# Performance work log

Measured on AMD Instinct MI355X. Metric: run time of the kernel, lower is better.

Reference implementation:

```python
import jax, jax.numpy as jnp
import numpy as np

# norse LIFCell default constants
DT = 1e-3
TAU_SYN_INV = 200.0
TAU_MEM_INV = 100.0
V_TH = 1.0
ALPHA = 100.0  # SuperSpike surrogate slope
BN_EPS = 1e-5
DECAY = 0.995

@jax.custom_vjp
def spike_fn(x):
    return (x > 0).astype(x.dtype)

def _spike_fwd(x):
    return spike_fn(x), x

def _spike_bwd(x, g):
    return (g / (ALPHA * jnp.abs(x) + 1.0) ** 2,)

spike_fn.defvjp(_spike_fwd, _spike_bwd)

def bn(x, g, b, m, v):
    return (x - m) * jax.lax.rsqrt(v + BN_EPS) * g + b

def lif_step(inp, v, i):
    # explicit Euler LIF update (v_leak = v_reset = 0)
    v_dec = v + DT * TAU_MEM_INV * (-v + i)
    i_dec = i * (1.0 - DT * TAU_SYN_INV)
    z = spike_fn(v_dec - V_TH)
    v_new = (1.0 - z) * v_dec
    i_new = i_dec + inp
    return z, v_new, i_new

def setup_inputs() -> dict:
    key = jax.random.key(0)
    ks = jax.random.split(key, 8)
    B, F, T = 2048, 512, 100
    H1, H2, H3, O = 1024, 512, 256, 2
    def xavier(k, fan_out, fan_in):
        lim = np.sqrt(6.0 / (fan_in + fan_out)).astype(np.float32)
        return jax.random.uniform(k, (fan_out, fan_in), jnp.float32, -lim, lim)
    def bn_params(k, n):
        return dict(g=jax.random.uniform(k, (n,), jnp.float32, 0.5, 1.5),
                    b=jnp.zeros((n,), jnp.float32),
                    m=jnp.zeros((n,), jnp.float32),
                    v=jnp.ones((n,), jnp.float32))
    bni = bn_params(ks[1], F); bn1 = bn_params(ks[2], H1)
    bn2 = bn_params(ks[3], H2); bn3 = bn_params(ks[4], H3)
    return {
        "x": jax.random.normal(ks[0], (B, F, T), jnp.float32),
        "bni_g": bni["g"], "bni_b": bni["b"], "bni_m": bni["m"], "bni_v": bni["v"],
        "W1": xavier(ks[5], H1, F), "b1": jnp.zeros((H1,), jnp.float32),
        "bn1_g": bn1["g"], "bn1_b": bn1["b"], "bn1_m": bn1["m"], "bn1_v": bn1["v"],
        "W2": xavier(ks[6], H2, H1), "b2": jnp.zeros((H2,), jnp.float32),
        "bn2_g": bn2["g"], "bn2_b": bn2["b"], "bn2_m": bn2["m"], "bn2_v": bn2["v"],
        "W3": xavier(ks[7], H3, H2), "b3": jnp.zeros((H3,), jnp.float32),
        "bn3_g": bn3["g"], "bn3_b": bn3["b"], "bn3_m": bn3["m"], "bn3_v": bn3["v"],
        "Wout": xavier(jax.random.fold_in(key, 99), O, H3),
        "bout": jnp.zeros((O,), jnp.float32),
    }

def reference(x, bni_g, bni_b, bni_m, bni_v,
              W1, b1, bn1_g, bn1_b, bn1_m, bn1_v,
              W2, b2, bn2_g, bn2_b, bn2_m, bn2_v,
              W3, b3, bn3_g, bn3_b, bn3_m, bn3_v,
              Wout, bout):
    B, F, T = x.shape
    O = Wout.shape[0]
    xs = jnp.moveaxis(x, 2, 0)  # (T, B, F)
    weights = DECAY ** jnp.arange(T - 1, -1, -1, dtype=x.dtype)  # (T,)

    def step(carry, inp):
        (v1, i1, v2, i2, v3, i3, vo, io, acc) = carry
        x_t, w = inp
        h = bn(x_t, bni_g, bni_b, bni_m, bni_v)
        c1 = bn(h @ W1.T + b1, bn1_g, bn1_b, bn1_m, bn1_v)
        z1, v1, i1 = lif_step(c1, v1, i1)
        c2 = bn(z1 @ W2.T + b2, bn2_g, bn2_b, bn2_m, bn2_v)
        z2, v2, i2 = lif_step(c2, v2, i2)
        c3 = bn(z2 @ W3.T + b3, bn3_g, bn3_b, bn3_m, bn3_v)
        z3, v3, i3 = lif_step(c3, v3, i3)
        co = z3 @ Wout.T + bout
        zo, vo, io = lif_step(co, vo, io)
        acc = acc + zo * w
        return (v1, i1, v2, i2, v3, i3, vo, io, acc), None

    zf = lambda n: jnp.zeros((B, n), x.dtype)
    init = (zf(W1.shape[0]), zf(W1.shape[0]), zf(W2.shape[0]), zf(W2.shape[0]),
            zf(W3.shape[0]), zf(W3.shape[0]), zf(O), zf(O), zf(O))
    carry, _ = jax.lax.scan(step, init, (xs, weights))
    return carry[-1]
```

## Files before the change

### kernel.cpp

```cpp
#include <hip/hip_runtime.h>
#include <cmath>

#define BATCH 2048
#define FDIM  512
#define TDIM  100
#define H1    1024
#define H2    512
#define H3    256
#define ODIM  2
#define TC    20
#define NCH   5
#define CHM   (TC * BATCH)

typedef __attribute__((ext_vector_type(8))) _Float16 f16x8;
typedef __attribute__((ext_vector_type(4))) _Float16 f16x4;
typedef __attribute__((ext_vector_type(4))) float f32x4;
typedef __attribute__((ext_vector_type(4))) int i32x4;

struct W20 { float w[TC]; };

__device__ __forceinline__ void gl16(const void* g, void* l) {
  __builtin_amdgcn_global_load_lds(
      (const __attribute__((address_space(1))) unsigned int*)g,
      (__attribute__((address_space(3))) unsigned int*)l, 16, 0, 0);
}

__device__ __forceinline__ void lif_update(float c, float& v, float& i, float& z) {
  float vd = v + 0.1f * (i - v);
  float id = 0.8f * i;
  z = (vd - 1.0f) > 0.0f ? 1.0f : 0.0f;
  v = (z != 0.0f) ? 0.0f : vd;
  i = id + c;
}

__global__ void zero_kernel(float* __restrict__ p, int n) {
  for (int i = blockIdx.x * blockDim.x + threadIdx.x; i < n; i += gridDim.x * blockDim.x)
    p[i] = 0.0f;
}

__global__ void tchunk_kernel(const float* __restrict__ x, _Float16* __restrict__ xp, int t0) {
  __shared__ float tile[64][21];
  const int b = blockIdx.y;
  const int f0 = blockIdx.x * 64;
  const int tid = threadIdx.x;
  {
    const int f = tid / 5, tq = tid % 5;
    float4 v = *reinterpret_cast<const float4*>(
        &x[(size_t)b * FDIM * TDIM + (size_t)(f0 + f) * TDIM + t0 + tq * 4]);
    tile[f][tq * 4 + 0] = v.x; tile[f][tq * 4 + 1] = v.y;
    tile[f][tq * 4 + 2] = v.z; tile[f][tq * 4 + 3] = v.w;
  }
  __syncthreads();
  {
    const int t = tid >> 4;
    const int fq = tid & 15;
    const size_t PS = (size_t)CHM * FDIM;
    f16x4 h, m;
    #pragma unroll
    for (int j = 0; j < 4; ++j) {
      float xa = tile[fq * 4 + j][t] * 64.0f;
      _Float16 hh = (_Float16)xa;
      float rm = (xa - (float)hh) * 4096.0f;
      h[j] = hh;
      m[j] = (_Float16)rm;
    }
    const size_t o = ((size_t)t * BATCH + b) * FDIM + f0 + fq * 4;
    *reinterpret_cast<f16x4*>(&xp[o])      = h;
    *reinterpret_cast<f16x4*>(&xp[PS + o]) = m;
  }
}

__global__ void fold1_f16(const float* __restrict__ W1, const float* __restrict__ b1,
                          const float* __restrict__ g1, const float* __restrict__ bb1,
                          const float* __restrict__ m1, const float* __restrict__ v1,
                          const float* __restrict__ gi, const float* __restrict__ bi,
                          const float* __restrict__ mi, const float* __restrict__ vi,
                          _Float16* __restrict__ W1p, float* __restrict__ s1,
                          float* __restrict__ e1) {
  __shared__ float swf[FDIM];
  __shared__ float red[8];
  __shared__ float bsw[1];
  const int j = blockIdx.x, tid = threadIdx.x;
  const float sg = g1[j] / sqrtf(v1[j] + 1e-5f);
  float part = 0.0f, pmax = 0.0f;
  for (int f = tid; f < FDIM; f += 256) {
    float si = gi[f] / sqrtf(vi[f] + 1e-5f);
    float h0 = bi[f] - mi[f] * si;
    float w  = W1[j * FDIM + f];
    part += w * h0;
    float wf = w * si * sg;
    swf[f] = wf;
    pmax = fmaxf(pmax, fabsf(wf));
  }
  #pragma unroll
  for (int s = 1; s < 64; s <<= 1) {
    part += __shfl_xor(part, s);
    pmax = fmaxf(pmax, __shfl_xor(pmax, s));
  }
  if ((tid & 63) == 0) { red[tid >> 6] = part; red[4 + (tid >> 6)] = pmax; }
  __syncthreads();
  if (tid == 0) {
    float d = red[0] + red[1] + red[2] + red[3];
    e1[j] = (d + b1[j] - m1[j]) * sg + bb1[j];
    float mx = fmaxf(fmaxf(red[4], red[5]), fmaxf(red[6], red[7]));
    int e = 0;
    if (mx > 0.0f) frexpf(mx, &e);
    s1[j] = exp2f((float)(e - 11));
    bsw[0] = exp2f((float)(5 - e));
  }
  __syncthreads();
  const float SW = bsw[0];
  const size_t PS = (size_t)H1 * FDIM;
  for (int f = tid; f < FDIM; f += 256) {
    float wa = swf[f] * SW;
    _Float16 wh = (_Float16)wa;
    float r = (wa - (float)wh) * 4096.0f;
    W1p[(size_t)j * FDIM + f]      = wh;
    W1p[PS + (size_t)j * FDIM + f] = (_Float16)r;
  }
}

__global__ void foldS_i8(const float* __restrict__ W, const float* __restrict__ b,
                         const float* __restrict__ g, const float* __restrict__ bb,
                         const float* __restrict__ m, const float* __restrict__ v,
                         signed char* __restrict__ Wq, float* __restrict__ qs,
                         float* __restrict__ e, int N, int K) {
  __shared__ float swf[1024];
  __shared__ float red[4];
  __shared__ int bse[1];
  const int j = blockIdx.x, tid = threadIdx.x;
  const float sg = g[j] / sqrtf(v[j] + 1e-5f);
  float pmax = 0.0f;
  for (int k = tid; k < K; k += 256) {
    float wf = W[(size_t)j * K + k] * sg;
    swf[k] = wf;
    pmax = fmaxf(pmax, fabsf(wf));
  }
  #pragma unroll
  for (int s = 1; s < 64; s <<= 1) pmax = fmaxf(pmax, __shfl_xor(pmax, s));
  if ((tid & 63) == 0) red[tid >> 6] = pmax;
  __syncthreads();
  if (tid == 0) {
    float mx = fmaxf(fmaxf(red[0], red[1]), fmaxf(red[2], red[3]));
    int ee = 0;
    if (mx > 0.0f) frexpf(mx, &ee);
    qs[j] = exp2f((float)(ee - 27));
    bse[0] = 27 - ee;
    e[j] = (b[j] - m[j]) * sg + bb[j];
  }
  __syncthreads();
  const double sc = ldexp(1.0, bse[0]);
  const size_t PS = (size_t)N * K;
  for (int k = tid; k < K; k += 256) {
    long D = llround((double)swf[k] * sc);
    #pragma unroll
    for (int p = 0; p < 3; p++) {
      int d = (int)(D & 127);
      if (d >= 64) d -= 128;
      Wq[(size_t)p * PS + (size_t)j * K + k] = (signed char)d;
      D = (D - d) >> 7;
    }
    Wq[3 * PS + (size_t)j * K + k] = (signed char)D;
  }
}

__global__ __launch_bounds__(256, 2)
void g1c_kernel(const _Float16* __restrict__ A, const _Float16* __restrict__ Wp,
                const float* __restrict__ s1, const float* __restrict__ e1,
                float* __restrict__ cOut)
{
  constexpr int BM = 128, BN = 64, K = FDIM, N = H1, BK = 64;
  constexpr int FR = 4, FC = 2, WTM = 64, WTN = 32;
  __shared__ __align__(16) _Float16 As[2][BM][BK];
  __shared__ __align__(16) _Float16 Bs[2][BN][BK];
  const int tid = threadIdx.x, lane = tid & 63, wid = tid >> 6;
  const int wr = wid >> 1, wc = wid & 1;
  const int l16 = lane & 15, lq = lane >> 4;
  const int bnk = blockIdx.x, bmk = blockIdx.y;
  const size_t APS = (size_t)CHM * FDIM;
  const size_t WPS = (size_t)N * K;
  const int lrow8 = lane >> 3, lslot = lane & 7;

  f32x4 accA[FR][FC] = {}, accB[FR][FC] = {};

  auto stage = [&](int it) {
    const int k0 = it * BK;
    #pragma unroll
    for (int q = 0; q < 8; ++q) {
      int i = q * 4 + wid;
      int s = i >> 4, r0 = (i & 15) * 8;
      int row = r0 + lrow8;
      int ss = lslot ^ (row & 7);
      gl16(A + (size_t)s * APS + (size_t)(bmk * BM + row) * K + k0 + ss * 8, &As[s][r0][0]);
    }
    #pragma unroll
    for (int q = 0; q < 4; ++q) {
      int i = q * 4 + wid;
      int s = i >> 3, r0 = (i & 7) * 8;
      int row = r0 + lrow8;
      int ss = lslot ^ (row & 7);
      gl16(Wp + (size_t)s * WPS + (size_t)(bnk * BN + row) * K + k0 + ss * 8, &Bs[s][r0][0]);
    }
  };

  auto loadA = [&](int kh, int s, int fr) -> f16x8 {
    int row = wr * WTM + fr * 16 + l16;
    int slot = ((kh << 2) | lq) ^ (row & 7);
    return *reinterpret_cast<const f16x8*>(&As[s][row][slot * 8]);
  };
  auto loadB = [&](int kh, int s, int fc) -> f16x8 {
    int row = wc * WTN + fc * 16 + l16;
    int slot = ((kh << 2) | lq) ^ (row & 7);
    return *reinterpret_cast<const f16x8*>(&Bs[s][row][slot * 8]);
  };

  stage(0);
  __syncthreads();
  constexpr int NK = K / BK;
  for (int it = 0; it < NK; ++it) {
    {
      f16x8 af[2][FR], bf[2][FC];
      #pragma unroll
      for (int s = 0; s < 2; ++s) {
        #pragma unroll
        for (int fr = 0; fr < FR; ++fr) af[s][fr] = loadA(0, s, fr);
        #pragma unroll
        for (int fc = 0; fc < FC; ++fc) bf[s][fc] = loadB(0, s, fc);
      }
      #pragma unroll
      for (int fr = 0; fr < FR; ++fr)
        #pragma unroll
        for (int fc = 0; fc < FC; ++fc) {
          accA[fr][fc] = __builtin_amdgcn_mfma_f32_16x16x32_f16(af[0][fr], bf[0][fc], accA[fr][fc], 0, 0, 0);
          accB[fr][fc] = __builtin_amdgcn_mfma_f32_16x16x32_f16(af[0][fr], bf[1][fc], accB[fr][fc], 0, 0, 0);
          accB[fr][fc] = __builtin_amdgcn_mfma_f32_16x16x32_f16(af[1][fr], bf[0][fc], accB[fr][fc], 0, 0, 0);
        }
    }
    {
      f16x8 af[2][FR], bf[2][FC];
      #pragma unroll
      for (int s = 0; s < 2; ++s) {
        #pragma unroll
        for (int fr = 0; fr < FR; ++fr) af[s][fr] = loadA(1, s, fr);
        #pragma unroll
        for (int fc = 0; fc < FC; ++fc) bf[s][fc] = loadB(1, s, fc);
      }
      __syncthreads();
      if (it + 1 < NK) stage(it + 1);
      #pragma unroll
      for (int fr = 0; fr < FR; ++fr)
        #pragma unroll
        for (int fc = 0; fc < FC; ++fc) {
          accA[fr][fc] = __builtin_amdgcn_mfma_f32_16x16x32_f16(af[0][fr], bf[0][fc], accA[fr][fc], 0, 0, 0);
          accB[fr][fc] = __builtin_amdgcn_mfma_f32_16x16x32_f16(af[0][fr], bf[1][fc], accB[fr][fc], 0, 0, 0);
          accB[fr][fc] = __builtin_amdgcn_mfma_f32_16x16x32_f16(af[1][fr], bf[0][fc], accB[fr][fc], 0, 0, 0);
        }
      __syncthreads();
    }
  }

  #pragma unroll
  for (int fc = 0; fc < FC; ++fc) {
    const int n = bnk * BN + wc * WTN + fc * 16 + l16;
    const float eb = e1[n], sn = s1[n];
    #pragma unroll
    for (int fr = 0; fr < FR; ++fr) {
      const int row0 = bmk * BM + wr * WTM + fr * 16 + lq * 4;
      #pragma unroll
      for (int r = 0; r < 4; ++r)
        cOut[(size_t)(row0 + r) * N + n] =
            sn * (accA[fr][fc][r] + 0.000244140625f * accB[fr][fc][r]) + eb;
    }
  }
}

template<int BM, int BN>
__global__ __launch_bounds__(256, 2)
void gSc_kernel(const signed char* __restrict__ A, const signed char* __restrict__ Wq,
                const float* __restrict__ qs, const float* __restrict__ eb_,
                float* __restrict__ cOut, const int N, const int K)
{
  constexpr int BKI = 128;
  constexpr int WTM = BM / 2, WTN = BN / 2, FR = WTM / 16, FC = WTN / 16;
  constexpr int RA = BM / 8, RB = BN / 8;
  __shared__ __align__(16) signed char As[BM][BKI];
  __shared__ __align__(16) signed char Bs[4][BN][BKI];
  const int tid = threadIdx.x, lane = tid & 63, wid = tid >> 6;
  const int wr = wid >> 1, wc = wid & 1;
  const int l16 = lane & 15, lq = lane >> 4;
  const int bnk = blockIdx.x, bmk = blockIdx.y;
  const size_t WPS = (size_t)N * K;
  const int lrow8 = lane >> 3, lslot = lane & 7;

  i32x4 acc[4][FR][FC] = {};

  auto stage = [&](int it) {
    const int k0 = it * BKI;
    #pragma unroll
    for (int q = 0; q < RA / 4; ++q) {
      int i = q * 4 + wid;
      int r0 = i * 8, row = r0 + lrow8;
      int ss = lslot ^ (row & 7);
      gl16(A + (size_t)(bmk * BM + row) * K + k0 + ss * 16, &As[r0][0]);
    }
    #pragma unroll
    for (int q = 0; q < RB; ++q) {
      int i = q * 4 + wid;
      int s = i / RB, r0 = (i % RB) * 8, row = r0 + lrow8;
      int ss = lslot ^ (row & 7);
      gl16(Wq + (size_t)s * WPS + (size_t)(bnk * BN + row) * K + k0 + ss * 16, &Bs[s][r0][0]);
    }
  };

  auto loadA = [&](int kh, int fr) -> i32x4 {
    int row = wr * WTM + fr * 16 + l16;
    int slot = ((kh << 2) | lq) ^ (row & 7);
    return *reinterpret_cast<const i32x4*>(&As[row][slot * 16]);
  };
  auto loadB = [&](int kh, int s, int fc) -> i32x4 {
    int row = wc * WTN + fc * 16 + l16;
    int slot = ((kh << 2) | lq) ^ (row & 7);
    return *reinterpret_cast<const i32x4*>(&Bs[s][row][slot * 16]);
  };

  stage(0);
  __syncthreads();
  const int NK = K / BKI;
  for (int it = 0; it < NK; ++it) {
    {
      i32x4 av[FR], bv[4][FC];
      #pragma unroll
      for (int fr = 0; fr < FR; ++fr) av[fr] = loadA(0, fr);
      #pragma unroll
      for (int s = 0; s < 4; ++s)
        #pragma unroll
        for (int fc = 0; fc < FC; ++fc) bv[s][fc] = loadB(0, s, fc);
      #pragma unroll
      for (int s = 0; s < 4; ++s)
        #pragma unroll
        for (int fr = 0; fr < FR; ++fr)
          #pragma unroll
          for (int fc = 0; fc < FC; ++fc)
            acc[s][fr][fc] = __builtin_amdgcn_mfma_i32_16x16x64_i8(av[fr], bv[s][fc], acc[s][fr][fc], 0, 0, 0);
    }
    {
      i32x4 av[FR], bv[4][FC];
      #pragma unroll
      for (int fr = 0; fr < FR; ++fr) av[fr] = loadA(1, fr);
      #pragma unroll
      for (int s = 0; s < 4; ++s)
        #pragma unroll
        for (int fc = 0; fc < FC; ++fc) bv[s][fc] = loadB(1, s, fc);
      __syncthreads();
      if (it + 1 < NK) stage(it + 1);
      #pragma unroll
      for (int s = 0; s < 4; ++s)
        #pragma unroll
        for (int fr = 0; fr < FR; ++fr)
          #pragma unroll
          for (int fc = 0; fc < FC; ++fc)
            acc[s][fr][fc] = __builtin_amdgcn_mfma_i32_16x16x64_i8(av[fr], bv[s][fc], acc[s][fr][fc], 0, 0, 0);
      __syncthreads();
    }
  }

  #pragma unroll
  for (int fc = 0; fc < FC; ++fc) {
    const int n = bnk * BN + wc * WTN + fc * 16 + l16;
    const float qv = qs[n], eb = eb_[n];
    #pragma unroll
    for (int fr = 0; fr < FR; ++fr) {
      const int row0 = bmk * BM + wr * WTM + fr * 16 + lq * 4;
      #pragma unroll
      for (int r = 0; r < 4; ++r) {
        int slo = acc[0][fr][fc][r] + (acc[1][fr][fc][r] << 7) + (acc[2][fr][fc][r] << 14);
        cOut[(size_t)(row0 + r) * N + n] =
            qv * fmaf(2097152.0f, (float)acc[3][fr][fc][r], (float)slo) + eb;
      }
    }
  }
}

__global__ void scan_lif_kernel(const float* __restrict__ c, float* __restrict__ vst,
                                float* __restrict__ ist, signed char* __restrict__ z,
                                int NN)
{
  const int i4 = (blockIdx.x * 256 + threadIdx.x) * 4;
  float4 v  = *reinterpret_cast<const float4*>(&vst[i4]);
  float4 ii = *reinterpret_cast<const float4*>(&ist[i4]);
  for (int t = 0; t < TC; ++t) {
    const size_t o = (size_t)t * NN + i4;
    float4 cc = *reinterpret_cast<const float4*>(&c[o]);
    float4 zz;
    lif_update(cc.x, v.x, ii.x, zz.x);
    lif_update(cc.y, v.y, ii.y, zz.y);
    lif_update(cc.z, v.z, ii.z, zz.z);
    lif_update(cc.w, v.w, ii.w, zz.w);
    unsigned pz = (zz.x != 0.f ? 1u : 0u) | (zz.y != 0.f ? 256u : 0u)
                | (zz.z != 0.f ? 65536u : 0u) | (zz.w != 0.f ? 16777216u : 0u);
    *reinterpret_cast<unsigned*>(&z[o]) = pz;
  }
  *reinterpret_cast<float4*>(&vst[i4]) = v;
  *reinterpret_cast<float4*>(&ist[i4]) = ii;
}

__global__ void outc_kernel(const signed char* __restrict__ z3, const float* __restrict__ Wout,
                            const float* __restrict__ bout, float* __restrict__ vo,
                            float* __restrict__ io, float* __restrict__ out, W20 wts)
{
  const int tid = threadIdx.x;
  const int ks = tid & 15, p = tid >> 4;
  const int o = p & 1, bl = p >> 1;
  const int b = blockIdx.x * 8 + bl;
  float wv[16];
  const float* wbase = Wout + (size_t)o * H3 + ks * 16;
  #pragma unroll
  for (int j = 0; j < 16; ++j) wv[j] = wbase[j];
  const float bo = bout[o];
  const int sidx = b * ODIM + o;
  float v = vo[sidx], i = io[sidx], accl = 0.0f;
  for (int t = 0; t < TC; ++t) {
    const signed char* zr = z3 + ((size_t)t * BATCH + b) * H3 + ks * 16;
    i32x4 zw = *reinterpret_cast<const i32x4*>(zr);
    float s = 0.0f;
    #pragma unroll
    for (int j = 0; j < 16; ++j)
      s = fmaf((float)((zw[j >> 2] >> ((j & 3) * 8)) & 1), wv[j], s);
    s += __shfl_xor(s, 1); s += __shfl_xor(s, 2);
    s += __shfl_xor(s, 4); s += __shfl_xor(s, 8);
    float zo;
    lif_update(s + bo, v, i, zo);
    accl += zo * wts.w[t];
  }
  if (ks == 0) { vo[sidx] = v; io[sidx] = i; out[sidx] += accl; }
}

__global__ void fold1_kernel(const float* __restrict__ W1, const float* __restrict__ b1,
                             const float* __restrict__ g1, const float* __restrict__ bb1,
                             const float* __restrict__ m1, const float* __restrict__ v1,
                             const float* __restrict__ gi, const float* __restrict__ bi,
                             const float* __restrict__ mi, const float* __restrict__ vi,
                             float* __restrict__ W1f, float* __restrict__ e1) {
  const int j = blockIdx.x;
  const int tid = threadIdx.x;
  const float sg = g1[j] / sqrtf(v1[j] + 1e-5f);
  float part = 0.0f;
  for (int f = tid; f < FDIM; f += 256) {
    float si = gi[f] / sqrtf(vi[f] + 1e-5f);
    float h0 = bi[f] - mi[f] * si;
    float w  = W1[j * FDIM + f];
    part += w * h0;
    W1f[j * FDIM + f] = w * si * sg;
  }
  #pragma unroll
  for (int m = 1; m < 64; m <<= 1) part += __shfl_xor(part, m);
  __shared__ float red[4];
  if ((tid & 63) == 0) red[tid >> 6] = part;
  __syncthreads();
  if (tid == 0) {
    float d = red[0] + red[1] + red[2] + red[3];
    e1[j] = (d + b1[j] - m1[j]) * sg + bb1[j];
  }
}

__global__ void foldS_kernel(const float* __restrict__ W, const float* __restrict__ b,
                             const float* __restrict__ g, const float* __restrict__ bb,
                             const float* __restrict__ m, const float* __restrict__ v,
                             float* __restrict__ Wf, float* __restrict__ e, int K) {
  const int j = blockIdx.x;
  const float sg = g[j] / sqrtf(v[j] + 1e-5f);
  for (int k = threadIdx.x; k < K; k += 256)
    Wf[j * K + k] = W[j * K + k] * sg;
  if (threadIdx.x == 0) e[j] = (b[j] - m[j]) * sg + bb[j];
}

template<int TM, int TN, bool CONTIG>
__global__ __launch_bounds__(256, 2)
void gemm_lif_kernel(const float* __restrict__ A, size_t ars, size_t acs,
                     const float* __restrict__ W, const float* __restrict__ ebias,
                     float* __restrict__ vst, float* __restrict__ ist,
                     float* __restrict__ zout, int N, int K)
{
  constexpr int BK = 16;
  constexpr int BM = 16 * TM;
  constexpr int BN = 16 * TN;
  __shared__ float As[BK][BM];
  __shared__ float Bs[BK][BN];
  const int tid = threadIdx.x;
  const int tx = tid & 15, ty = tid >> 4;
  const int bn = blockIdx.x, bm = blockIdx.y;
  const float* Ablk = A + (size_t)bm * BM * ars;
  const float* Wblk = W + (size_t)bn * BN * (size_t)K;

  float acc[TM][TN];
  #pragma unroll
  for (int r = 0; r < TM; r++)
    #pragma unroll
    for (int c = 0; c < TN; c++) acc[r][c] = 0.0f;

  for (int k0 = 0; k0 < K; k0 += BK) {
    if (CONTIG) {
      constexpr int A4 = BM * BK / 4;
      #pragma unroll
      for (int q = 0; q < A4 / 256; q++) {
        int idx = q * 256 + tid;
        int r = idx >> 2;
        int kq = (idx & 3) << 2;
        float4 val = *reinterpret_cast<const float4*>(Ablk + (size_t)r * ars + (size_t)(k0 + kq));
        As[kq + 0][r] = val.x; As[kq + 1][r] = val.y;
        As[kq + 2][r] = val.z; As[kq + 3][r] = val.w;
      }
    } else {
      #pragma unroll
      for (int q = 0; q < BM * BK / 256; q++) {
        int idx = q * 256 + tid;
        int r = idx >> 4;
        int kk = idx & 15;
        As[kk][r] = Ablk[(size_t)r * ars + (size_t)(k0 + kk) * acs];
      }
    }
    {
      int n  = tid >> 2;
      int kq = (tid & 3) << 2;
      float4 val = *reinterpret_cast<const float4*>(Wblk + (size_t)n * K + (size_t)(k0 + kq));
      Bs[kq + 0][n] = val.x; Bs[kq + 1][n] = val.y;
      Bs[kq + 2][n] = val.z; Bs[kq + 3][n] = val.w;
    }
    __syncthreads();
    #pragma unroll
    for (int kk = 0; kk < BK; kk++) {
      float a[TM], bv[TN];
      const float4* ap = reinterpret_cast<const float4*>(&As[kk][ty * TM]);
      *reinterpret_cast<float4*>(&a[0]) = ap[0];
      if (TM == 8) *reinterpret_cast<float4*>(&a[4]) = ap[1];
      *reinterpret_cast<float4*>(&bv[0]) = *reinterpret_cast<const float4*>(&Bs[kk][tx * TN]);
      #pragma unroll
      for (int r = 0; r < TM; r++)
        #pragma unroll
        for (int c = 0; c < TN; c++)
          acc[r][c] = fmaf(a[r], bv[c], acc[r][c]);
    }
    __syncthreads();
  }

  const int n0 = bn * BN + tx * TN;
  const float4 ev = *reinterpret_cast<const float4*>(ebias + n0);
  #pragma unroll
  for (int r = 0; r < TM; r++) {
    const int brow = bm * BM + ty * TM + r;
    const size_t idx = (size_t)brow * N + n0;
    float c0 = acc[r][0] + ev.x;
    float c1 = acc[r][1] + ev.y;
    float c2 = acc[r][2] + ev.z;
    float c3 = acc[r][3] + ev.w;
    float4 vv = *reinterpret_cast<const float4*>(vst + idx);
    float4 ii = *reinterpret_cast<const float4*>(ist + idx);
    float4 zz;
    lif_update(c0, vv.x, ii.x, zz.x);
    lif_update(c1, vv.y, ii.y, zz.y);
    lif_update(c2, vv.z, ii.z, zz.z);
    lif_update(c3, vv.w, ii.w, zz.w);
    *reinterpret_cast<float4*>(zout + idx) = zz;
    *reinterpret_cast<float4*>(vst  + idx) = vv;
    *reinterpret_cast<float4*>(ist  + idx) = ii;
  }
}

__global__ void out_kernel(const float* __restrict__ z3, const float* __restrict__ Wout,
                           const float* __restrict__ bout, float* __restrict__ vo,
                           float* __restrict__ io, float* __restrict__ acc, float wt) {
  const int idx = blockIdx.x * 256 + threadIdx.x;
  if (idx >= BATCH * ODIM) return;
  const int b = idx >> 1, o = idx & 1;
  const float4* zr = reinterpret_cast<const float4*>(z3 + (size_t)b * H3);
  const float4* wr = reinterpret_cast<const float4*>(Wout + o * H3);
  float s = 0.0f;
  #pragma unroll 4
  for (int k = 0; k < H3 / 4; k++) {
    float4 zv = zr[k], wv = wr[k];
    s += zv.x * wv.x + zv.y * wv.y + zv.z * wv.z + zv.w * wv.w;
  }
  float cin = s + bout[o];
  float v = vo[idx], i = io[idx], z;
  lif_update(cin, v, i, z);
  vo[idx] = v; io[idx] = i;
  acc[idx] += z * wt;
}

extern "C" void kernel_launch(void* const* d_in, const int* in_sizes, int n_in,
                              void* d_out, int out_size, void* d_ws, size_t ws_size,
                              hipStream_t stream) {
  const float* x     = (const float*)d_in[0];
  const float* bni_g = (const float*)d_in[1];
  const float* bni_b = (const float*)d_in[2];
  const float* bni_m = (const float*)d_in[3];
  const float* bni_v = (const float*)d_in[4];
  const float* W1    = (const float*)d_in[5];
  const float* b1    = (const float*)d_in[6];
  const float* bn1_g = (const float*)d_in[7];
  const float* bn1_b = (const float*)d_in[8];
  const float* bn1_m = (const float*)d_in[9];
  const float* bn1_v = (const float*)d_in[10];
  const float* W2    = (const float*)d_in[11];
  const float* b2    = (const float*)d_in[12];
  const float* bn2_g = (const float*)d_in[13];
  const float* bn2_b = (const float*)d_in[14];
  const float* bn2_m = (const float*)d_in[15];
  const float* bn2_v = (const float*)d_in[16];
  const float* W3    = (const float*)d_in[17];
  const float* b3    = (const float*)d_in[18];
  const float* bn3_g = (const float*)d_in[19];
  const float* bn3_b = (const float*)d_in[20];
  const float* bn3_m = (const float*)d_in[21];
  const float* bn3_v = (const float*)d_in[22];
  const float* Wout  = (const float*)d_in[23];
  const float* bout  = (const float*)d_in[24];
  float* out = (float*)d_out;

  float* ws = (float*)d_ws;
  size_t off = 0;
  auto alloc = [&](size_t n) { float* p = ws + off; off += n; return p; };

  float* e1 = alloc(H1);
  float* e2 = alloc(H2);
  float* e3 = alloc(H3);
  float* s1 = alloc(H1);
  float* q2 = alloc(H2);
  float* q3 = alloc(H3);
  float* v1 = alloc((size_t)BATCH * H1);
  float* i1 = alloc((size_t)BATCH * H1);
  float* v2 = alloc((size_t)BATCH * H2);
  float* i2 = alloc((size_t)BATCH * H2);
  float* v3 = alloc((size_t)BATCH * H3);
  float* i3 = alloc((size_t)BATCH * H3);
  float* vo = alloc((size_t)BATCH * ODIM);
  float* io = alloc((size_t)BATCH * ODIM);
  float* cbuf = alloc((size_t)CHM * H1);
  _Float16* hs = (_Float16*)(ws + off);
  size_t hoff = 0;
  _Float16* W1p = hs; hoff += (size_t)2 * H1 * FDIM;
  _Float16* Xp_c = hs + hoff; hoff += (size_t)2 * CHM * FDIM;
  signed char* za = (signed char*)Xp_c;
  signed char* bs = (signed char*)(hs + hoff);
  size_t boff = 0;
  signed char* W2q = bs + boff; boff += (size_t)4 * H2 * H1;
  signed char* W3q = bs + boff; boff += (size_t)4 * H3 * H2;
  const size_t needed = off * sizeof(float) + hoff * sizeof(_Float16) + boff;

  const int nstate = BATCH * (2 * H1 + 2 * H2 + 2 * H3 + 2 * ODIM);

  if (ws_size >= needed) {
    zero_kernel<<<2048, 256, 0, stream>>>(v1, nstate);
    zero_kernel<<<16, 256, 0, stream>>>(out, BATCH * ODIM);

    fold1_f16<<<H1, 256, 0, stream>>>(W1, b1, bn1_g, bn1_b, bn1_m, bn1_v,
                                      bni_g, bni_b, bni_m, bni_v, W1p, s1, e1);
    foldS_i8<<<H2, 256, 0, stream>>>(W2, b2, bn2_g, bn2_b, bn2_m, bn2_v, W2q, q2, e2, H2, H1);
    foldS_i8<<<H3, 256, 0, stream>>>(W3, b3, bn3_g, bn3_b, bn3_m, bn3_v, W3q, q3, e3, H3, H2);

    for (int ch = 0; ch < NCH; ++ch) {
      const int t0 = ch * TC;
      tchunk_kernel<<<dim3(FDIM / 64, BATCH), 320, 0, stream>>>(x, Xp_c, t0);
      g1c_kernel<<<dim3(H1 / 64, CHM / 128), 256, 0, stream>>>(Xp_c, W1p, s1, e1, cbuf);
      scan_lif_kernel<<<BATCH * H1 / 1024, 256, 0, stream>>>(cbuf, v1, i1, za, BATCH * H1);
      gSc_kernel<64, 64><<<dim3(H2 / 64, CHM / 64), 256, 0, stream>>>(za, W2q, q2, e2, cbuf, H2, H1);
      scan_lif_kernel<<<BATCH * H2 / 1024, 256, 0, stream>>>(cbuf, v2, i2, za, BATCH * H2);
      gSc_kernel<64, 32><<<dim3(H3 / 32, CHM / 64), 256, 0, stream>>>(za, W3q, q3, e3, cbuf, H3, H2);
      scan_lif_kernel<<<BATCH * H3 / 1024, 256, 0, stream>>>(cbuf, v3, i3, za, BATCH * H3);
      W20 wts;
      for (int tt = 0; tt < TC; ++tt)
        wts.w[tt] = (float)std::pow(0.995, (double)(TDIM - 1 - (t0 + tt)));
      outc_kernel<<<BATCH / 8, 256, 0, stream>>>(za, Wout, bout, vo, io, out, wts);
    }
    return;
  }

  off = 0;
  float* W1f = alloc((size_t)H1 * FDIM);
  float* W2f = alloc((size_t)H2 * H1);
  float* W3f = alloc((size_t)H3 * H2);
  float* fe1 = alloc(H1);
  float* fe2 = alloc(H2);
  float* fe3 = alloc(H3);
  float* fv1 = alloc((size_t)BATCH * H1);
  float* fi1 = alloc((size_t)BATCH * H1);
  float* fv2 = alloc((size_t)BATCH * H2);
  float* fi2 = alloc((size_t)BATCH * H2);
  float* fv3 = alloc((size_t)BATCH * H3);
  float* fi3 = alloc((size_t)BATCH * H3);
  float* fvo = alloc((size_t)BATCH * ODIM);
  float* fio = alloc((size_t)BATCH * ODIM);
  float* fz1 = alloc((size_t)BATCH * H1);
  float* fz2 = alloc((size_t)BATCH * H2);
  float* fz3 = alloc((size_t)BATCH * H3);

  zero_kernel<<<2048, 256, 0, stream>>>(fv1, nstate);
  zero_kernel<<<16, 256, 0, stream>>>(out, BATCH * ODIM);

  fold1_kernel<<<H1, 256, 0, stream>>>(W1, b1, bn1_g, bn1_b, bn1_m, bn1_v,
                                       bni_g, bni_b, bni_m, bni_v, W1f, fe1);
  foldS_kernel<<<H2, 256, 0, stream>>>(W2, b2, bn2_g, bn2_b, bn2_m, bn2_v, W2f, fe2, H1);
  foldS_kernel<<<H3, 256, 0, stream>>>(W3, b3, bn3_g, bn3_b, bn3_m, bn3_v, W3f, fe3, H2);

  const dim3 fg1(H1 / 64, BATCH / 128);
  const dim3 fg2(H2 / 64, BATCH / 64);
  const dim3 fg3(H3 / 64, BATCH / 64);

  for (int t = 0; t < TDIM; t++) {
    gemm_lif_kernel<8, 4, false><<<fg1, 256, 0, stream>>>(
        x + t, (size_t)FDIM * TDIM, TDIM, W1f, fe1, fv1, fi1, fz1, H1, FDIM);
    gemm_lif_kernel<4, 4, true><<<fg2, 256, 0, stream>>>(fz1, H1, 1, W2f, fe2, fv2, fi2, fz2, H2, H1);
    gemm_lif_kernel<4, 4, true><<<fg3, 256, 0, stream>>>(fz2, H2, 1, W3f, fe3, fv3, fi3, fz3, H3, H2);
    float wt = (float)std::pow(0.995, (double)(TDIM - 1 - t));
    out_kernel<<<BATCH * ODIM / 256, 256, 0, stream>>>(fz3, Wout, bout, fvo, fio, out, wt);
  }
}
```

Before: 2.015 ms.

## Software-pipeline layers across time chunks with merged wavefront GEMM and scan launches

Restructures the per-chunk sequence of eight launches into a skewed wavefront. Each step runs a combined GEMM kernel (layer-1 on chunk k, layer-2 on k-1, layer-3 on k-2) and a combined scan kernel that also transposes the next input chunk into a double buffer. The layer-3 scan is fused with the output LIF readout, which removes the z3 buffer and the separate outc kernel. This cuts launch count and fills the GPU with independent work from several layers at once. In exchange it uses separate c and z buffers per layer plus a double-buffered Xp, increasing workspace, and runs two extra pipeline fill and drain steps where many blocks exit immediately.

```diff
diff --git a/kernel.cpp b/kernel.cpp
--- a/kernel.cpp
+++ b/kernel.cpp
@@ -11,6 +11,7 @@
 #define TC    20
 #define NCH   5
 #define CHM   (TC * BATCH)
+#define XPL   ((size_t)2 * CHM * FDIM)
 
 typedef __attribute__((ext_vector_type(8))) _Float16 f16x8;
 typedef __attribute__((ext_vector_type(4))) _Float16 f16x4;
@@ -38,23 +39,24 @@
     p[i] = 0.0f;
 }
 
-__global__ void tchunk_kernel(const float* __restrict__ x, _Float16* __restrict__ xp, int t0) {
+__device__ __forceinline__ void tchunk_body(const float* __restrict__ x,
+                                            _Float16* __restrict__ xp, int t0, int r) {
   __shared__ float tile[64][21];
-  const int b = blockIdx.y;
-  const int f0 = blockIdx.x * 64;
+  const int b = r >> 3;
+  const int f0 = (r & 7) * 64;
   const int tid = threadIdx.x;
-  {
-    const int f = tid / 5, tq = tid % 5;
+  for (int idx = tid; idx < 320; idx += 256) {
+    const int f = idx / 5, tq = idx % 5;
     float4 v = *reinterpret_cast<const float4*>(
         &x[(size_t)b * FDIM * TDIM + (size_t)(f0 + f) * TDIM + t0 + tq * 4]);
     tile[f][tq * 4 + 0] = v.x; tile[f][tq * 4 + 1] = v.y;
     tile[f][tq * 4 + 2] = v.z; tile[f][tq * 4 + 3] = v.w;
   }
   __syncthreads();
-  {
-    const int t = tid >> 4;
-    const int fq = tid & 15;
-    const size_t PS = (size_t)CHM * FDIM;
+  const size_t PS = (size_t)CHM * FDIM;
+  for (int idx = tid; idx < 320; idx += 256) {
+    const int t = idx >> 4;
+    const int fq = idx & 15;
     f16x4 h, m;
     #pragma unroll
     for (int j = 0; j < 4; ++j) {
@@ -68,6 +70,10 @@
     *reinterpret_cast<f16x4*>(&xp[o])      = h;
     *reinterpret_cast<f16x4*>(&xp[PS + o]) = m;
   }
+}
+
+__global__ void tchunk_kernel(const float* __restrict__ x, _Float16* __restrict__ xp, int t0) {
+  tchunk_body(x, xp, t0, blockIdx.x);
 }
 
 __global__ void fold1_f16(const float* __restrict__ W1, const float* __restrict__ b1,
@@ -164,19 +170,19 @@
   }
 }
 
-__global__ __launch_bounds__(256, 2)
-void g1c_kernel(const _Float16* __restrict__ A, const _Float16* __restrict__ Wp,
-                const float* __restrict__ s1, const float* __restrict__ e1,
-                float* __restrict__ cOut)
+__device__ __forceinline__ void g1_body(unsigned char* smem, int bnk, int bmk,
+    const _Float16* __restrict__ A, const _Float16* __restrict__ Wp,
+    const float* __restrict__ s1, const float* __restrict__ e1, float* __restrict__ cOut)
 {
   constexpr int BM = 128, BN = 64, K = FDIM, N = H1, BK = 64;
   constexpr int FR = 4, FC = 2, WTM = 64, WTN = 32;
-  __shared__ __align__(16) _Float16 As[2][BM][BK];
-  __shared__ __align__(16) _Float16 Bs[2][BN][BK];
+  typedef _Float16 (*F16A)[BM][BK];
+  typedef _Float16 (*F16B)[BN][BK];
+  F16A As = (F16A)smem;
+  F16B Bs = (F16B)(smem + 2 * BM * BK * sizeof(_Float16));
   const int tid = threadIdx.x, lane = tid & 63, wid = tid >> 6;
   const int wr = wid >> 1, wc = wid & 1;
   const int l16 = lane & 15, lq = lane >> 4;
-  const int bnk = blockIdx.x, bmk = blockIdx.y;
   const size_t APS = (size_t)CHM * FDIM;
   const size_t WPS = (size_t)N * K;
   const int lrow8 = lane >> 3, lslot = lane & 7;
@@ -275,20 +281,21 @@
 }
 
 template<int BM, int BN>
-__global__ __launch_bounds__(256, 2)
-void gSc_kernel(const signed char* __restrict__ A, const signed char* __restrict__ Wq,
-                const float* __restrict__ qs, const float* __restrict__ eb_,
-                float* __restrict__ cOut, const int N, const int K)
+__device__ __forceinline__ void gS_body(unsigned char* smem, int bnk, int bmk,
+    const signed char* __restrict__ A, const signed char* __restrict__ Wq,
+    const float* __restrict__ qs, const float* __restrict__ eb_,
+    float* __restrict__ cOut, const int N, const int K)
 {
   constexpr int BKI = 128;
   constexpr int WTM = BM / 2, WTN = BN / 2, FR = WTM / 16, FC = WTN / 16;
   constexpr int RA = BM / 8, RB = BN / 8;
-  __shared__ __align__(16) signed char As[BM][BKI];
-  __shared__ __align__(16) signed char Bs[4][BN][BKI];
+  typedef signed char (*I8A)[BKI];
+  typedef signed char (*I8B)[BN][BKI];
+  I8A As = (I8A)smem;
+  I8B Bs = (I8B)(smem + BM * BKI);
   const int tid = threadIdx.x, lane = tid & 63, wid = tid >> 6;
   const int wr = wid >> 1, wc = wid & 1;
   const int l16 = lane & 15, lq = lane >> 4;
-  const int bnk = blockIdx.x, bmk = blockIdx.y;
   const size_t WPS = (size_t)N * K;
   const int lrow8 = lane >> 3, lslot = lane & 7;
 
@@ -381,11 +388,11 @@
   }
 }
 
-__global__ void scan_lif_kernel(const float* __restrict__ c, float* __restrict__ vst,
-                                float* __restrict__ ist, signed char* __restrict__ z,
-                                int NN)
+__device__ __forceinline__ void scan_body(const float* __restrict__ c, float* __restrict__ vst,
+                                          float* __restrict__ ist, signed char* __restrict__ z,
+                                          int NN, int r)
 {
-  const int i4 = (blockIdx.x * 256 + threadIdx.x) * 4;
+  const int i4 = (r * 256 + threadIdx.x) * 4;
   float4 v  = *reinterpret_cast<const float4*>(&vst[i4]);
   float4 ii = *reinterpret_cast<const float4*>(&ist[i4]);
   for (int t = 0; t < TC; ++t) {
@@ -404,35 +411,117 @@
   *reinterpret_cast<float4*>(&ist[i4]) = ii;
 }
 
-__global__ void outc_kernel(const signed char* __restrict__ z3, const float* __restrict__ Wout,
-                            const float* __restrict__ bout, float* __restrict__ vo,
-                            float* __restrict__ io, float* __restrict__ out, W20 wts)
+__device__ __forceinline__ void scan3out_body(const float* __restrict__ c3,
+    float* __restrict__ v3, float* __restrict__ i3,
+    const float* __restrict__ Wout, const float* __restrict__ bout,
+    float* __restrict__ vo, float* __restrict__ io, float* __restrict__ out,
+    const W20& wts, int r)
 {
-  const int tid = threadIdx.x;
-  const int ks = tid & 15, p = tid >> 4;
-  const int o = p & 1, bl = p >> 1;
-  const int b = blockIdx.x * 8 + bl;
-  float wv[16];
-  const float* wbase = Wout + (size_t)o * H3 + ks * 16;
+  const int lane = threadIdx.x & 63, wv = threadIdx.x >> 6;
+  const int b = r * 4 + wv;
+  const int n0 = lane * 4;
+  const size_t sidx = (size_t)b * H3 + n0;
+  float4 v  = *reinterpret_cast<const float4*>(&v3[sidx]);
+  float4 ii = *reinterpret_cast<const float4*>(&i3[sidx]);
+  const float4 w0 = *reinterpret_cast<const float4*>(&Wout[n0]);
+  const float4 w1 = *reinterpret_cast<const float4*>(&Wout[H3 + n0]);
+  const float bo0 = bout[0], bo1 = bout[1];
+  const int oidx = b * ODIM;
+  float vo0 = vo[oidx], io0 = io[oidx], vo1 = vo[oidx + 1], io1 = io[oidx + 1];
+  float acc0 = 0.0f, acc1 = 0.0f;
   #pragma unroll
-  for (int j = 0; j < 16; ++j) wv[j] = wbase[j];
-  const float bo = bout[o];
-  const int sidx = b * ODIM + o;
-  float v = vo[sidx], i = io[sidx], accl = 0.0f;
   for (int t = 0; t < TC; ++t) {
-    const signed char* zr = z3 + ((size_t)t * BATCH + b) * H3 + ks * 16;
-    i32x4 zw = *reinterpret_cast<const i32x4*>(zr);
-    float s = 0.0f;
-    #pragma unroll
-    for (int j = 0; j < 16; ++j)
-      s = fmaf((float)((zw[j >> 2] >> ((j & 3) * 8)) & 1), wv[j], s);
-    s += __shfl_xor(s, 1); s += __shfl_xor(s, 2);
-    s += __shfl_xor(s, 4); s += __shfl_xor(s, 8);
-    float zo;
-    lif_update(s + bo, v, i, zo);
-    accl += zo * wts.w[t];
-  }
-  if (ks == 0) { vo[sidx] = v; io[sidx] = i; out[sidx] += accl; }
+    const size_t o = ((size_t)t * BATCH + b) * H3 + n0;
+    float4 cc = *reinterpret_cast<const float4*>(&c3[o]);
+    float4 zz;
+    lif_update(cc.x, v.x, ii.x, zz.x);
+    lif_update(cc.y, v.y, ii.y, zz.y);
+    lif_update(cc.z, v.z, ii.z, zz.z);
+    lif_update(cc.w, v.w, ii.w, zz.w);
+    float s0 = fmaf(zz.x, w0.x, fmaf(zz.y, w0.y, fmaf(zz.z, w0.z, zz.w * w0.w)));
+    float s1 = fmaf(zz.x, w1.x, fmaf(zz.y, w1.y, fmaf(zz.z, w1.z, zz.w * w1.w)));
+    #pragma unroll
+    for (int m = 1; m < 64; m <<= 1) {
+      s0 += __shfl_xor(s0, m);
+      s1 += __shfl_xor(s1, m);
+    }
+    float zo0, zo1;
+    lif_update(s0 + bo0, vo0, io0, zo0);
+    lif_update(s1 + bo1, vo1, io1, zo1);
+    acc0 += zo0 * wts.w[t];
+    acc1 += zo1 * wts.w[t];
+  }
+  *reinterpret_cast<float4*>(&v3[sidx]) = v;
+  *reinterpret_cast<float4*>(&i3[sidx]) = ii;
+  if (lane == 0) {
+    vo[oidx] = vo0; io[oidx] = io0;
+    vo[oidx + 1] = vo1; io[oidx + 1] = io1;
+    out[oidx] += acc0; out[oidx + 1] += acc1;
+  }
+}
+
+#define NB_G1 5120
+#define NB_G2 5120
+#define NB_G3 5120
+__global__ __launch_bounds__(256, 2)
+void stepA(const _Float16* __restrict__ Xp, const _Float16* __restrict__ W1p,
+           const float* __restrict__ s1, const float* __restrict__ e1, float* __restrict__ c1,
+           const signed char* __restrict__ z1, const signed char* __restrict__ W2q,
+           const float* __restrict__ q2, const float* __restrict__ e2, float* __restrict__ c2,
+           const signed char* __restrict__ z2, const signed char* __restrict__ W3q,
+           const float* __restrict__ q3, const float* __restrict__ e3, float* __restrict__ c3,
+           int k)
+{
+  __shared__ __align__(16) unsigned char smem[49152];
+  const int r = blockIdx.x;
+  if (r < NB_G1) {
+    if (k >= NCH) return;
+    g1_body(smem, r & 15, r >> 4, Xp + (size_t)(k & 1) * XPL, W1p, s1, e1, c1);
+  } else if (r < NB_G1 + NB_G2) {
+    const int kk = k - 1;
+    if (kk < 0 || kk >= NCH) return;
+    const int r2 = r - NB_G1;
+    gS_body<64, 64>(smem, r2 & 7, r2 >> 3, z1, W2q, q2, e2, c2, H2, H1);
+  } else {
+    const int kk = k - 2;
+    if (kk < 0 || kk >= NCH) return;
+    const int r3 = r - NB_G1 - NB_G2;
+    gS_body<64, 32>(smem, r3 & 7, r3 >> 3, z2, W3q, q3, e3, c3, H3, H2);
+  }
+}
+
+#define NB_S1 2048
+#define NB_S2 1024
+#define NB_S3 512
+#define NB_TK 16384
+__global__ __launch_bounds__(256, 4)
+void stepB(const float* __restrict__ c1, float* __restrict__ v1, float* __restrict__ i1,
+           signed char* __restrict__ z1,
+           const float* __restrict__ c2, float* __restrict__ v2, float* __restrict__ i2,
+           signed char* __restrict__ z2,
+           const float* __restrict__ c3, float* __restrict__ v3, float* __restrict__ i3,
+           const float* __restrict__ Wout, const float* __restrict__ bout,
+           float* __restrict__ vo, float* __restrict__ io, float* __restrict__ out,
+           const float* __restrict__ x, _Float16* __restrict__ Xp,
+           int k, W20 wts)
+{
+  const int r = blockIdx.x;
+  if (r < NB_S1) {
+    if (k >= NCH) return;
+    scan_body(c1, v1, i1, z1, BATCH * H1, r);
+  } else if (r < NB_S1 + NB_S2) {
+    const int kk = k - 1;
+    if (kk < 0 || kk >= NCH) return;
+    scan_body(c2, v2, i2, z2, BATCH * H2, r - NB_S1);
+  } else if (r < NB_S1 + NB_S2 + NB_S3) {
+    const int kk = k - 2;
+    if (kk < 0 || kk >= NCH) return;
+    scan3out_body(c3, v3, i3, Wout, bout, vo, io, out, wts, r - NB_S1 - NB_S2);
+  } else {
+    const int kk = k + 1;
+    if (kk >= NCH) return;
+    tchunk_body(x, Xp + (size_t)(kk & 1) * XPL, kk * TC, r - NB_S1 - NB_S2 - NB_S3);
+  }
 }
 
 __global__ void fold1_kernel(const float* __restrict__ W1, const float* __restrict__ b1,
@@ -635,16 +724,19 @@
   float* i3 = alloc((size_t)BATCH * H3);
   float* vo = alloc((size_t)BATCH * ODIM);
   float* io = alloc((size_t)BATCH * ODIM);
-  float* cbuf = alloc((size_t)CHM * H1);
+  float* c1 = alloc((size_t)CHM * H1);
+  float* c2 = alloc((size_t)CHM * H2);
+  float* c3 = alloc((size_t)CHM * H3);
   _Float16* hs = (_Float16*)(ws + off);
   size_t hoff = 0;
   _Float16* W1p = hs; hoff += (size_t)2 * H1 * FDIM;
-  _Float16* Xp_c = hs + hoff; hoff += (size_t)2 * CHM * FDIM;
-  signed char* za = (signed char*)Xp_c;
+  _Float16* Xp  = hs + hoff; hoff += 2 * XPL;
   signed char* bs = (signed char*)(hs + hoff);
   size_t boff = 0;
   signed char* W2q = bs + boff; boff += (size_t)4 * H2 * H1;
   signed char* W3q = bs + boff; boff += (size_t)4 * H3 * H2;
+  signed char* z1  = bs + boff; boff += (size_t)CHM * H1;
+  signed char* z2  = bs + boff; boff += (size_t)CHM * H2;
   const size_t needed = off * sizeof(float) + hoff * sizeof(_Float16) + boff;
 
   const int nstate = BATCH * (2 * H1 + 2 * H2 + 2 * H3 + 2 * ODIM);
@@ -657,20 +749,19 @@
                                       bni_g, bni_b, bni_m, bni_v, W1p, s1, e1);
     foldS_i8<<<H2, 256, 0, stream>>>(W2, b2, bn2_g, bn2_b, bn2_m, bn2_v, W2q, q2, e2, H2, H1);
     foldS_i8<<<H3, 256, 0, stream>>>(W3, b3, bn3_g, bn3_b, bn3_m, bn3_v, W3q, q3, e3, H3, H2);
-
-    for (int ch = 0; ch < NCH; ++ch) {
-      const int t0 = ch * TC;
-      tchunk_kernel<<<dim3(FDIM / 64, BATCH), 320, 0, stream>>>(x, Xp_c, t0);
-      g1c_kernel<<<dim3(H1 / 64, CHM / 128), 256, 0, stream>>>(Xp_c, W1p, s1, e1, cbuf);
-      scan_lif_kernel<<<BATCH * H1 / 1024, 256, 0, stream>>>(cbuf, v1, i1, za, BATCH * H1);
-      gSc_kernel<64, 64><<<dim3(H2 / 64, CHM / 64), 256, 0, stream>>>(za, W2q, q2, e2, cbuf, H2, H1);
-      scan_lif_kernel<<<BATCH * H2 / 1024, 256, 0, stream>>>(cbuf, v2, i2, za, BATCH * H2);
-      gSc_kernel<64, 32><<<dim3(H3 / 32, CHM / 64), 256, 0, stream>>>(za, W3q, q3, e3, cbuf, H3, H2);
-      scan_lif_kernel<<<BATCH * H3 / 1024, 256, 0, stream>>>(cbuf, v3, i3, za, BATCH * H3);
-      W20 wts;
-      for (int tt = 0; tt < TC; ++tt)
-        wts.w[tt] = (float)std::pow(0.995, (double)(TDIM - 1 - (t0 + tt)));
-      outc_kernel<<<BATCH / 8, 256, 0, stream>>>(za, Wout, bout, vo, io, out, wts);
+    tchunk_kernel<<<NB_TK, 256, 0, stream>>>(x, Xp, 0);
+
+    for (int k = 0; k <= NCH + 1; ++k) {
+      stepA<<<NB_G1 + NB_G2 + NB_G3, 256, 0, stream>>>(
+          Xp, W1p, s1, e1, c1, z1, W2q, q2, e2, c2, z2, W3q, q3, e3, c3, k);
+      W20 wts{};
+      const int cc = k - 2;
+      if (cc >= 0 && cc < NCH)
+        for (int tt = 0; tt < TC; ++tt)
+          wts.w[tt] = (float)std::pow(0.995, (double)(TDIM - 1 - (cc * TC + tt)));
+      stepB<<<NB_S1 + NB_S2 + NB_S3 + NB_TK, 256, 0, stream>>>(
+          c1, v1, i1, z1, c2, v2, i2, z2, c3, v3, i3,
+          Wout, bout, vo, io, out, x, Xp, k, wts);
     }
     return;
   }
```

New measurement: 2.251 ms. 1.12x slower.

## Process all timesteps in one pass and fuse layer-3 scan with output

Applied to the files above, without the earlier changes.

Removes the 5-chunk time loop so each GEMM and LIF scan runs over all 100 timesteps at once. Scans start from zero state, so persistent v/i buffers and the zeroing kernels go away. The layer-3 LIF scan is fused with the output projection and output LIF into a single kernel. This cuts kernel launches and state round-trips and gives larger GEMM grids. In exchange it needs a much larger workspace for full-length intermediates, which loses last-level-cache residency and can drop to the slow fallback path if the workspace is too small.

```diff
diff --git a/kernel.cpp b/kernel.cpp
--- a/kernel.cpp
+++ b/kernel.cpp
@@ -8,16 +8,14 @@
 #define H2    512
 #define H3    256
 #define ODIM  2
-#define TC    20
-#define NCH   5
-#define CHM   (TC * BATCH)
+#define M_ALL (TDIM * BATCH)
 
 typedef __attribute__((ext_vector_type(8))) _Float16 f16x8;
 typedef __attribute__((ext_vector_type(4))) _Float16 f16x4;
 typedef __attribute__((ext_vector_type(4))) float f32x4;
 typedef __attribute__((ext_vector_type(4))) int i32x4;
 
-struct W20 { float w[TC]; };
+struct W100 { float w[TDIM]; };
 
 __device__ __forceinline__ void gl16(const void* g, void* l) {
   __builtin_amdgcn_global_load_lds(
@@ -38,23 +36,22 @@
     p[i] = 0.0f;
 }
 
-__global__ void tchunk_kernel(const float* __restrict__ x, _Float16* __restrict__ xp, int t0) {
-  __shared__ float tile[64][21];
-  const int b = blockIdx.y;
+__global__ void tchunk_kernel(const float* __restrict__ x, _Float16* __restrict__ xp) {
+  __shared__ float tile[64][105];
   const int f0 = blockIdx.x * 64;
+  const int b  = blockIdx.y;
   const int tid = threadIdx.x;
-  {
-    const int f = tid / 5, tq = tid % 5;
-    float4 v = *reinterpret_cast<const float4*>(
-        &x[(size_t)b * FDIM * TDIM + (size_t)(f0 + f) * TDIM + t0 + tq * 4]);
-    tile[f][tq * 4 + 0] = v.x; tile[f][tq * 4 + 1] = v.y;
-    tile[f][tq * 4 + 2] = v.z; tile[f][tq * 4 + 3] = v.w;
+  const size_t xb = (size_t)b * FDIM * TDIM;
+  for (int idx = tid; idx < 1600; idx += 256) {
+    const int f = idx / 25, q = idx % 25;
+    float4 v = *reinterpret_cast<const float4*>(&x[xb + (size_t)(f0 + f) * TDIM + q * 4]);
+    tile[f][q * 4 + 0] = v.x; tile[f][q * 4 + 1] = v.y;
+    tile[f][q * 4 + 2] = v.z; tile[f][q * 4 + 3] = v.w;
   }
   __syncthreads();
-  {
-    const int t = tid >> 4;
-    const int fq = tid & 15;
-    const size_t PS = (size_t)CHM * FDIM;
+  const size_t PS = (size_t)M_ALL * FDIM;
+  for (int idx = tid; idx < 1600; idx += 256) {
+    const int t = idx >> 4, fq = idx & 15;
     f16x4 h, m;
     #pragma unroll
     for (int j = 0; j < 4; ++j) {
@@ -177,7 +174,7 @@
   const int wr = wid >> 1, wc = wid & 1;
   const int l16 = lane & 15, lq = lane >> 4;
   const int bnk = blockIdx.x, bmk = blockIdx.y;
-  const size_t APS = (size_t)CHM * FDIM;
+  const size_t APS = (size_t)M_ALL * FDIM;
   const size_t WPS = (size_t)N * K;
   const int lrow8 = lane >> 3, lslot = lane & 7;
 
@@ -381,14 +378,13 @@
   }
 }
 
-__global__ void scan_lif_kernel(const float* __restrict__ c, float* __restrict__ vst,
-                                float* __restrict__ ist, signed char* __restrict__ z,
+__global__ void scan_lif_kernel(const float* __restrict__ c, signed char* __restrict__ z,
                                 int NN)
 {
   const int i4 = (blockIdx.x * 256 + threadIdx.x) * 4;
-  float4 v  = *reinterpret_cast<const float4*>(&vst[i4]);
-  float4 ii = *reinterpret_cast<const float4*>(&ist[i4]);
-  for (int t = 0; t < TC; ++t) {
+  float4 v  = make_float4(0.f, 0.f, 0.f, 0.f);
+  float4 ii = make_float4(0.f, 0.f, 0.f, 0.f);
+  for (int t = 0; t < TDIM; ++t) {
     const size_t o = (size_t)t * NN + i4;
     float4 cc = *reinterpret_cast<const float4*>(&c[o]);
     float4 zz;
@@ -400,39 +396,48 @@
                 | (zz.z != 0.f ? 65536u : 0u) | (zz.w != 0.f ? 16777216u : 0u);
     *reinterpret_cast<unsigned*>(&z[o]) = pz;
   }
-  *reinterpret_cast<float4*>(&vst[i4]) = v;
-  *reinterpret_cast<float4*>(&ist[i4]) = ii;
-}
-
-__global__ void outc_kernel(const signed char* __restrict__ z3, const float* __restrict__ Wout,
-                            const float* __restrict__ bout, float* __restrict__ vo,
-                            float* __restrict__ io, float* __restrict__ out, W20 wts)
+}
+
+__global__ void scan3out_kernel(const float* __restrict__ c3,
+                                const float* __restrict__ Wout, const float* __restrict__ bout,
+                                float* __restrict__ out, W100 wts)
 {
-  const int tid = threadIdx.x;
-  const int ks = tid & 15, p = tid >> 4;
-  const int o = p & 1, bl = p >> 1;
-  const int b = blockIdx.x * 8 + bl;
-  float wv[16];
-  const float* wbase = Wout + (size_t)o * H3 + ks * 16;
-  #pragma unroll
-  for (int j = 0; j < 16; ++j) wv[j] = wbase[j];
-  const float bo = bout[o];
-  const int sidx = b * ODIM + o;
-  float v = vo[sidx], i = io[sidx], accl = 0.0f;
-  for (int t = 0; t < TC; ++t) {
-    const signed char* zr = z3 + ((size_t)t * BATCH + b) * H3 + ks * 16;
-    i32x4 zw = *reinterpret_cast<const i32x4*>(zr);
-    float s = 0.0f;
-    #pragma unroll
-    for (int j = 0; j < 16; ++j)
-      s = fmaf((float)((zw[j >> 2] >> ((j & 3) * 8)) & 1), wv[j], s);
-    s += __shfl_xor(s, 1); s += __shfl_xor(s, 2);
-    s += __shfl_xor(s, 4); s += __shfl_xor(s, 8);
-    float zo;
-    lif_update(s + bo, v, i, zo);
-    accl += zo * wts.w[t];
-  }
-  if (ks == 0) { vo[sidx] = v; io[sidx] = i; out[sidx] += accl; }
+  const int lane = threadIdx.x & 63, wv = threadIdx.x >> 6;
+  const int b = blockIdx.x * 4 + wv;
+  const int n0 = lane * 4;
+  float4 v  = make_float4(0.f, 0.f, 0.f, 0.f);
+  float4 ii = make_float4(0.f, 0.f, 0.f, 0.f);
+  const float4 w0 = *reinterpret_cast<const float4*>(&Wout[n0]);
+  const float4 w1 = *reinterpret_cast<const float4*>(&Wout[H3 + n0]);
+  const float bo0 = bout[0], bo1 = bout[1];
+  float vo0 = 0.f, io0 = 0.f, vo1 = 0.f, io1 = 0.f;
+  float acc0 = 0.0f, acc1 = 0.0f;
+  for (int t = 0; t < TDIM; ++t) {
+    const size_t o = ((size_t)t * BATCH + b) * H3 + n0;
+    float4 cc = *reinterpret_cast<const float4*>(&c3[o]);
+    float4 zz;
+    lif_update(cc.x, v.x, ii.x, zz.x);
+    lif_update(cc.y, v.y, ii.y, zz.y);
+    lif_update(cc.z, v.z, ii.z, zz.z);
+    lif_update(cc.w, v.w, ii.w, zz.w);
+    float s0 = fmaf(zz.x, w0.x, fmaf(zz.y, w0.y, fmaf(zz.z, w0.z, zz.w * w0.w)));
+    float s1 = fmaf(zz.x, w1.x, fmaf(zz.y, w1.y, fmaf(zz.z, w1.z, zz.w * w1.w)));
+    #pragma unroll
+    for (int m = 1; m < 64; m <<= 1) {
+      s0 += __shfl_xor(s0, m);
+      s1 += __shfl_xor(s1, m);
+    }
+    float zo0, zo1;
+    lif_update(s0 + bo0, vo0, io0, zo0);
+    lif_update(s1 + bo1, vo1, io1, zo1);
+    acc0 += zo0 * wts.w[t];
+    acc1 += zo1 * wts.w[t];
+  }
+  if (lane == 0) {
+    const int oidx = b * ODIM;
+    out[oidx]     = acc0;
+    out[oidx + 1] = acc1;
+  }
 }
 
 __global__ void fold1_kernel(const float* __restrict__ W1, const float* __restrict__ b1,
@@ -627,51 +632,42 @@
   float* s1 = alloc(H1);
   float* q2 = alloc(H2);
   float* q3 = alloc(H3);
-  float* v1 = alloc((size_t)BATCH * H1);
-  float* i1 = alloc((size_t)BATCH * H1);
-  float* v2 = alloc((size_t)BATCH * H2);
-  float* i2 = alloc((size_t)BATCH * H2);
-  float* v3 = alloc((size_t)BATCH * H3);
-  float* i3 = alloc((size_t)BATCH * H3);
-  float* vo = alloc((size_t)BATCH * ODIM);
-  float* io = alloc((size_t)BATCH * ODIM);
-  float* cbuf = alloc((size_t)CHM * H1);
-  _Float16* hs = (_Float16*)(ws + off);
-  size_t hoff = 0;
-  _Float16* W1p = hs; hoff += (size_t)2 * H1 * FDIM;
-  _Float16* Xp_c = hs + hoff; hoff += (size_t)2 * CHM * FDIM;
-  signed char* za = (signed char*)Xp_c;
-  signed char* bs = (signed char*)(hs + hoff);
+  unsigned char* base = (unsigned char*)(ws + off);
   size_t boff = 0;
-  signed char* W2q = bs + boff; boff += (size_t)4 * H2 * H1;
-  signed char* W3q = bs + boff; boff += (size_t)4 * H3 * H2;
-  const size_t needed = off * sizeof(float) + hoff * sizeof(_Float16) + boff;
-
-  const int nstate = BATCH * (2 * H1 + 2 * H2 + 2 * H3 + 2 * ODIM);
+  auto carve = [&](size_t bytes) {
+    void* p = base + boff;
+    boff += (bytes + 255) & ~(size_t)255;
+    return p;
+  };
+  _Float16* W1p   = (_Float16*)carve((size_t)2 * H1 * FDIM * 2);
+  signed char* W2q = (signed char*)carve((size_t)4 * H2 * H1);
+  signed char* W3q = (signed char*)carve((size_t)4 * H3 * H2);
+  signed char* z1  = (signed char*)carve((size_t)M_ALL * H1);
+  signed char* z2  = (signed char*)carve((size_t)M_ALL * H2);
+  void* regionA = carve((size_t)2 * M_ALL * FDIM * 2);
+  void* regionB = carve((size_t)M_ALL * H1 * 4);
+  _Float16* Xp = (_Float16*)regionA;
+  float* c2    = (float*)regionA;
+  float* c1    = (float*)regionB;
+  float* c3    = (float*)regionB;
+  const size_t needed = off * sizeof(float) + boff;
 
   if (ws_size >= needed) {
-    zero_kernel<<<2048, 256, 0, stream>>>(v1, nstate);
-    zero_kernel<<<16, 256, 0, stream>>>(out, BATCH * ODIM);
-
     fold1_f16<<<H1, 256, 0, stream>>>(W1, b1, bn1_g, bn1_b, bn1_m, bn1_v,
                                       bni_g, bni_b, bni_m, bni_v, W1p, s1, e1);
     foldS_i8<<<H2, 256, 0, stream>>>(W2, b2, bn2_g, bn2_b, bn2_m, bn2_v, W2q, q2, e2, H2, H1);
     foldS_i8<<<H3, 256, 0, stream>>>(W3, b3, bn3_g, bn3_b, bn3_m, bn3_v, W3q, q3, e3, H3, H2);
 
-    for (int ch = 0; ch < NCH; ++ch) {
-      const int t0 = ch * TC;
-      tchunk_kernel<<<dim3(FDIM / 64, BATCH), 320, 0, stream>>>(x, Xp_c, t0);
-      g1c_kernel<<<dim3(H1 / 64, CHM / 128), 256, 0, stream>>>(Xp_c, W1p, s1, e1, cbuf);
-      scan_lif_kernel<<<BATCH * H1 / 1024, 256, 0, stream>>>(cbuf, v1, i1, za, BATCH * H1);
-      gSc_kernel<64, 64><<<dim3(H2 / 64, CHM / 64), 256, 0, stream>>>(za, W2q, q2, e2, cbuf, H2, H1);
-      scan_lif_kernel<<<BATCH * H2 / 1024, 256, 0, stream>>>(cbuf, v2, i2, za, BATCH * H2);
-      gSc_kernel<64, 32><<<dim3(H3 / 32, CHM / 64), 256, 0, stream>>>(za, W3q, q3, e3, cbuf, H3, H2);
-      scan_lif_kernel<<<BATCH * H3 / 1024, 256, 0, stream>>>(cbuf, v3, i3, za, BATCH * H3);
-      W20 wts;
-      for (int tt = 0; tt < TC; ++tt)
-        wts.w[tt] = (float)std::pow(0.995, (double)(TDIM - 1 - (t0 + tt)));
-      outc_kernel<<<BATCH / 8, 256, 0, stream>>>(za, Wout, bout, vo, io, out, wts);
-    }
+    tchunk_kernel<<<dim3(FDIM / 64, BATCH), 256, 0, stream>>>(x, Xp);
+    g1c_kernel<<<dim3(H1 / 64, M_ALL / 128), 256, 0, stream>>>(Xp, W1p, s1, e1, c1);
+    scan_lif_kernel<<<BATCH * H1 / 1024, 256, 0, stream>>>(c1, z1, BATCH * H1);
+    gSc_kernel<64, 64><<<dim3(H2 / 64, M_ALL / 64), 256, 0, stream>>>(z1, W2q, q2, e2, c2, H2, H1);
+    scan_lif_kernel<<<BATCH * H2 / 1024, 256, 0, stream>>>(c2, z2, BATCH * H2);
+    gSc_kernel<64, 32><<<dim3(H3 / 32, M_ALL / 64), 256, 0, stream>>>(z2, W3q, q3, e3, c3, H3, H2);
+    W100 wts;
+    for (int t = 0; t < TDIM; ++t)
+      wts.w[t] = (float)std::pow(0.995, (double)(TDIM - 1 - t));
+    scan3out_kernel<<<BATCH / 4, 256, 0, stream>>>(c3, Wout, bout, out, wts);
     return;
   }
 
@@ -694,6 +690,7 @@
   float* fz2 = alloc((size_t)BATCH * H2);
   float* fz3 = alloc((size_t)BATCH * H3);
 
+  const int nstate = BATCH * (2 * H1 + 2 * H2 + 2 * H3 + 2 * ODIM);
   zero_kernel<<<2048, 256, 0, stream>>>(fv1, nstate);
   zero_kernel<<<16, 256, 0, stream>>>(out, BATCH * ODIM);
 
```

Measured after the change: 1.972 ms. -2.1%, faster.
